# Kernel tuning notes

Measured on AMD Instinct MI355X. Metric: run time of the kernel, lower is better.

Reference implementation:

```python
import jax, jax.numpy as jnp
import numpy as np

TOP_K = 2

def setup_inputs() -> dict:
    key = jax.random.key(0)
    ks = jax.random.split(key, 5)
    B, S, H, F, E = 2, 1024, 2048, 4096, 8
    scale_h = 1.0 / np.sqrt(H)
    scale_f = 1.0 / np.sqrt(F)
    return {
        "hidden_states": jax.random.normal(ks[0], (B, S, H), dtype=jnp.float32),
        # nn.Linear weight layout is [out, in]
        "gate_w": jax.random.normal(ks[1], (E, H), dtype=jnp.float32) * scale_h,
        "w_gate": jax.random.normal(ks[2], (E, F, H), dtype=jnp.float32) * scale_h,
        "w_up": jax.random.normal(ks[3], (E, F, H), dtype=jnp.float32) * scale_h,
        "w_down": jax.random.normal(ks[4], (E, H, F), dtype=jnp.float32) * scale_f,
    }

def reference(hidden_states, gate_w, w_gate, w_up, w_down):
    B, S, H = hidden_states.shape
    E = gate_w.shape[0]
    x = hidden_states.reshape(-1, H)                     # [T, H]
    T = x.shape[0]
    # Router: softmax -> top-k -> renormalize
    router_logits = x @ gate_w.T                         # [T, E]
    routing_weights = jax.nn.softmax(router_logits, axis=-1)
    topk_w, topk_i = jax.lax.top_k(routing_weights, TOP_K)  # [T, k]
    topk_w = topk_w / jnp.sum(topk_w, axis=-1, keepdims=True)
    # Dense [T, E] combine weights (zero for non-selected experts);
    # equivalent math to the per-expert gather/scatter loop.
    dense_w = jnp.zeros((T, E), dtype=x.dtype).at[
        jnp.arange(T)[:, None], topk_i].set(topk_w)
    # SwiGLU experts, batched over E (grouped GEMM expressed densely)
    g = jnp.einsum('th,efh->tef', x, w_gate)             # [T, E, F]
    u = jnp.einsum('th,efh->tef', x, w_up)               # [T, E, F]
    h = jax.nn.silu(g) * u                               # [T, E, F]
    y = jnp.einsum('tef,ehf->teh', h, w_down)            # [T, E, H]
    out = jnp.einsum('te,teh->th', dense_w, y)           # [T, H]
    return out.reshape(B, S, H)
```

## Files before the change

### kernel.cpp

```cpp
#include <hip/hip_runtime.h>
#include <hip/hip_bf16.h>


#define T_TOK 2048
#define H_DIM 2048
#define F_DIM 4096
#define E_NUM 8
#define NPAIR (T_TOK * 2)

typedef __attribute__((ext_vector_type(8))) short short8;
typedef __attribute__((ext_vector_type(4))) float f32x4;

__device__ __forceinline__ unsigned short f2bf(float f) {
    unsigned u = __builtin_bit_cast(unsigned, f);
    u = (u + 0x7FFFu + ((u >> 16) & 1u)) >> 16;
    return (unsigned short)u;
}

__device__ __forceinline__ uint4 pack8(float4 a, float4 b) {
    uint4 o;
    o.x = f2bf(a.x) | ((unsigned)f2bf(a.y) << 16);
    o.y = f2bf(a.z) | ((unsigned)f2bf(a.w) << 16);
    o.z = f2bf(b.x) | ((unsigned)f2bf(b.y) << 16);
    o.w = f2bf(b.z) | ((unsigned)f2bf(b.w) << 16);
    return o;
}

__global__ void k_cvt_x(const float* __restrict__ x, ushort* __restrict__ xb) {
    int i = blockIdx.x * blockDim.x + threadIdx.x;
    const float4* p = (const float4*)x + (size_t)i * 2;
    ((uint4*)xb)[i] = pack8(p[0], p[1]);
}

__global__ void k_router(const float* __restrict__ x, const float* __restrict__ gw,
                         int2* __restrict__ eidx, float2* __restrict__ ew,
                         int* __restrict__ cnt) {
    int t = blockIdx.x * 4 + (threadIdx.x >> 6);
    int lane = threadIdx.x & 63;
    const float* xr = x + (size_t)t * H_DIM;
    float l[E_NUM];
    #pragma unroll
    for (int e = 0; e < E_NUM; e++) {
        const float* wr = gw + (size_t)e * H_DIM;
        float acc = 0.f;
        for (int i = lane; i < H_DIM; i += 64) acc += xr[i] * wr[i];
        #pragma unroll
        for (int o = 32; o; o >>= 1) acc += __shfl_xor(acc, o);
        l[e] = acc;
    }
    if (lane == 0) {
        int e0 = 0;
        #pragma unroll
        for (int e = 1; e < E_NUM; e++) if (l[e] > l[e0]) e0 = e;
        int e1 = -1;
        #pragma unroll
        for (int e = 0; e < E_NUM; e++) {
            if (e == e0) continue;
            if (e1 < 0 || l[e] > l[e1]) e1 = e;
        }
        float s1 = expf(l[e1] - l[e0]);
        float w0 = 1.f / (1.f + s1);
        float w1 = s1 * w0;
        eidx[t] = make_int2(e0, e1);
        ew[t]   = make_float2(w0, w1);
        atomicAdd(&cnt[e0], 1);
        atomicAdd(&cnt[e1], 1);
    }
}

__global__ void k_off(const int* __restrict__ cnt, int* __restrict__ off,
                      int* __restrict__ cnt2) {
    if (threadIdx.x == 0) {
        int s = 0;
        for (int e = 0; e < E_NUM; e++) { off[e] = s; s += cnt[e]; cnt2[e] = 0; }
        off[E_NUM] = s;
    }
}

__global__ void k_fill(const int2* __restrict__ eidx, const float2* __restrict__ ew,
                       const int* __restrict__ off, int* __restrict__ cnt2,
                       int* __restrict__ ptok, int2* __restrict__ inv) {
    int t = blockIdx.x * blockDim.x + threadIdx.x;
    if (t >= T_TOK) return;
    int2 e = eidx[t];
    int p0 = off[e.x] + atomicAdd(&cnt2[e.x], 1);
    ptok[p0] = t;
    int p1 = off[e.y] + atomicAdd(&cnt2[e.y], 1);
    ptok[p1] = t;
    inv[t] = make_int2(p0, p1);
}

__global__ __launch_bounds__(512, 4) void k_gemm1(
        const ushort* __restrict__ xb, const float* __restrict__ wg,
        const float* __restrict__ wu, const int* __restrict__ ptok,
        const int* __restrict__ off, ushort* __restrict__ hbuf) {
    __shared__ __align__(16) ushort As[256 * 64];
    __shared__ __align__(16) ushort Bg[64 * 64];
    __shared__ __align__(16) ushort Bu[64 * 64];

    int e = blockIdx.y >> 4, mt = blockIdx.y & 15;
    int base = off[e], ne = off[e + 1] - base;
    int row0 = mt * 256;
    if (row0 >= ne) return;
    int nb = blockIdx.x * 64;

    int tid = threadIdx.x;
    int wv = tid >> 6, l = tid & 63;
    int lr = l & 15, lk = l >> 4;
    int wm = wv >> 1, wn = wv & 1;

    int arow = tid >> 1, ah = (tid & 1) * 4;
    int p = base + min(row0 + arow, ne - 1);
    const ushort* xrow = xb + (size_t)ptok[p] * H_DIM;
    int asw = (arow & 7) << 4;
    int ao[4];
    #pragma unroll
    for (int j = 0; j < 4; j++)
        ao[j] = arow * 64 + ((((ah + j) * 16) ^ asw) >> 1);

    int brow = tid >> 3, bs = tid & 7;
    const float* wgrow = wg + ((size_t)e * F_DIM + nb + brow) * H_DIM + bs * 8;
    const float* wurow = wu + ((size_t)e * F_DIM + nb + brow) * H_DIM + bs * 8;
    int bo = brow * 64 + (((bs * 16) ^ ((brow & 7) << 4)) >> 1);

    int rsw = (lr & 7) << 4;

    f32x4 accg[4][2] = {}; f32x4 accu[4][2] = {};

    for (int kb = 0; kb < H_DIM; kb += 64) {
        __syncthreads();
        #pragma unroll
        for (int j = 0; j < 4; j++)
            *(uint4*)(&As[ao[j]]) = *(const uint4*)(xrow + kb + (ah + j) * 8);
        float4 g0 = *(const float4*)(wgrow + kb);
        float4 g1 = *(const float4*)(wgrow + kb + 4);
        *(uint4*)(&Bg[bo]) = pack8(g0, g1);
        float4 u0 = *(const float4*)(wurow + kb);
        float4 u1 = *(const float4*)(wurow + kb + 4);
        *(uint4*)(&Bu[bo]) = pack8(u0, u1);
        __syncthreads();

        #pragma unroll
        for (int kk = 0; kk < 2; kk++) {
            int kby = kk * 64 + lk * 16;
            short8 a[4];
            #pragma unroll
            for (int m = 0; m < 4; m++) {
                int row = wm * 64 + m * 16 + lr;
                a[m] = *(const short8*)(&As[(row * 128 + (kby ^ rsw)) >> 1]);
            }
            #pragma unroll
            for (int n = 0; n < 2; n++) {
                int rowb = wn * 32 + n * 16 + lr;
                int boff = (rowb * 128 + (kby ^ rsw)) >> 1;
                short8 bg8 = *(const short8*)(&Bg[boff]);
                short8 bu8 = *(const short8*)(&Bu[boff]);
                #pragma unroll
                for (int m = 0; m < 4; m++) {
                    accg[m][n] = __builtin_amdgcn_mfma_f32_16x16x32_bf16(a[m], bg8, accg[m][n], 0, 0, 0);
                    accu[m][n] = __builtin_amdgcn_mfma_f32_16x16x32_bf16(a[m], bu8, accu[m][n], 0, 0, 0);
                }
            }
        }
    }

    #pragma unroll
    for (int m = 0; m < 4; m++) {
        #pragma unroll
        for (int r = 0; r < 4; r++) {
            int lrow = wm * 64 + m * 16 + lk * 4 + r;
            if (row0 + lrow < ne) {
                size_t rb = (size_t)(base + row0 + lrow) * F_DIM + nb;
                #pragma unroll
                for (int n = 0; n < 2; n++) {
                    float g = accg[m][n][r], u = accu[m][n][r];
                    float hv = g / (1.f + __expf(-g)) * u;
                    hbuf[rb + wn * 32 + n * 16 + lr] = f2bf(hv);
                }
            }
        }
    }
}

__global__ __launch_bounds__(512, 2) void k_gemm2(
        const ushort* __restrict__ hbuf, const float* __restrict__ wd,
        const int* __restrict__ off, float* __restrict__ ybuf) {
    __shared__ __align__(16) ushort As[256 * 64];
    __shared__ __align__(16) ushort Bs[128 * 64];

    int e = blockIdx.y >> 3, mt = blockIdx.y & 7;
    int base = off[e], ne = off[e + 1] - base;
    int row0 = mt * 256;
    if (row0 >= ne) return;
    int nb = blockIdx.x * 128;

    int tid = threadIdx.x;
    int wv = tid >> 6, l = tid & 63;
    int lr = l & 15, lk = l >> 4;
    int wm = wv >> 1, wn = wv & 1;

    int arow = tid >> 1, ah = (tid & 1) * 4;
    int p = base + min(row0 + arow, ne - 1);
    const ushort* hrow = hbuf + (size_t)p * F_DIM;
    int asw = (arow & 7) << 4;
    int ao[4];
    #pragma unroll
    for (int j = 0; j < 4; j++)
        ao[j] = arow * 64 + ((((ah + j) * 16) ^ asw) >> 1);

    int brow = tid >> 2, bs = tid & 3;
    const float* wdrow = wd + ((size_t)e * H_DIM + nb + brow) * F_DIM + bs * 16;
    int bsw = (brow & 7) << 4;
    int bo0 = brow * 64 + (((bs * 32) ^ bsw) >> 1);
    int bo1 = brow * 64 + (((bs * 32 + 16) ^ bsw) >> 1);

    int rsw = (lr & 7) << 4;

    f32x4 acc[4][4] = {};

    for (int kb = 0; kb < F_DIM; kb += 64) {
        __syncthreads();
        #pragma unroll
        for (int j = 0; j < 4; j++)
            *(uint4*)(&As[ao[j]]) = *(const uint4*)(hrow + kb + (ah + j) * 8);
        float4 b0 = *(const float4*)(wdrow + kb);
        float4 b1 = *(const float4*)(wdrow + kb + 4);
        float4 b2 = *(const float4*)(wdrow + kb + 8);
        float4 b3 = *(const float4*)(wdrow + kb + 12);
        *(uint4*)(&Bs[bo0]) = pack8(b0, b1);
        *(uint4*)(&Bs[bo1]) = pack8(b2, b3);
        __syncthreads();

        #pragma unroll
        for (int kk = 0; kk < 2; kk++) {
            int kby = kk * 64 + lk * 16;
            short8 a[4];
            #pragma unroll
            for (int m = 0; m < 4; m++) {
                int row = wm * 64 + m * 16 + lr;
                a[m] = *(const short8*)(&As[(row * 128 + (kby ^ rsw)) >> 1]);
            }
            #pragma unroll
            for (int n = 0; n < 4; n++) {
                int rowb = wn * 64 + n * 16 + lr;
                short8 b8 = *(const short8*)(&Bs[(rowb * 128 + (kby ^ rsw)) >> 1]);
                #pragma unroll
                for (int m = 0; m < 4; m++)
                    acc[m][n] = __builtin_amdgcn_mfma_f32_16x16x32_bf16(a[m], b8, acc[m][n], 0, 0, 0);
            }
        }
    }

    #pragma unroll
    for (int m = 0; m < 4; m++) {
        #pragma unroll
        for (int r = 0; r < 4; r++) {
            int lrow = wm * 64 + m * 16 + lk * 4 + r;
            if (row0 + lrow < ne) {
                float* yrow = ybuf + (size_t)(base + row0 + lrow) * H_DIM + nb;
                #pragma unroll
                for (int n = 0; n < 4; n++)
                    yrow[wn * 64 + n * 16 + lr] = acc[m][n][r];
            }
        }
    }
}

__global__ void k_combine(const float* __restrict__ ybuf,
                          const float2* __restrict__ ew,
                          const int2* __restrict__ inv,
                          float* __restrict__ out) {
    int t = blockIdx.x;
    float2 w = ew[t];
    int2 pp = inv[t];
    const float4* y0 = (const float4*)(ybuf + (size_t)pp.x * H_DIM);
    const float4* y1 = (const float4*)(ybuf + (size_t)pp.y * H_DIM);
    float4* o = (float4*)(out + (size_t)t * H_DIM);
    for (int j = threadIdx.x; j < H_DIM / 4; j += blockDim.x) {
        float4 a = y0[j], b = y1[j];
        float4 r;
        r.x = w.x * a.x + w.y * b.x;
        r.y = w.x * a.y + w.y * b.y;
        r.z = w.x * a.z + w.y * b.z;
        r.w = w.x * a.w + w.y * b.w;
        o[j] = r;
    }
}

extern "C" void kernel_launch(void* const* d_in, const int* in_sizes, int n_in,
                              void* d_out, int out_size, void* d_ws, size_t ws_size,
                              hipStream_t stream) {
    const float* x  = (const float*)d_in[0];
    const float* gw = (const float*)d_in[1];
    const float* wg = (const float*)d_in[2];
    const float* wu = (const float*)d_in[3];
    const float* wd = (const float*)d_in[4];
    float* out = (float*)d_out;

    char* ws = (char*)d_ws;
    size_t o = 0;
    ushort* xb   = (ushort*)(ws + o); o += (size_t)T_TOK * H_DIM * 2;
    ushort* hbuf = (ushort*)(ws + o); o += (size_t)NPAIR * F_DIM * 2;
    float*  ybuf = (float*) (ws + o); o += (size_t)NPAIR * H_DIM * 4;
    int*    ptok = (int*)   (ws + o); o += NPAIR * 4;
    int2*   eidx = (int2*)  (ws + o); o += T_TOK * 8;
    float2* ew   = (float2*)(ws + o); o += T_TOK * 8;
    int2*   inv  = (int2*)  (ws + o); o += T_TOK * 8;
    int*    cnt  = (int*)   (ws + o); o += 256;
    int*    cnt2 = (int*)   (ws + o); o += 256;
    int*    off  = (int*)   (ws + o); o += 256;

    hipMemsetAsync(cnt, 0, 256, stream);

    k_cvt_x <<<T_TOK * H_DIM / 8 / 256, 256, 0, stream>>>(x, xb);
    k_router<<<T_TOK / 4, 256, 0, stream>>>(x, gw, eidx, ew, cnt);
    k_off   <<<1, 64, 0, stream>>>(cnt, off, cnt2);
    k_fill  <<<T_TOK / 256, 256, 0, stream>>>(eidx, ew, off, cnt2, ptok, inv);

    dim3 g1(F_DIM / 64, E_NUM * 16);
    k_gemm1<<<g1, 512, 0, stream>>>(xb, wg, wu, ptok, off, hbuf);
    dim3 g2(H_DIM / 128, E_NUM * 8);
    k_gemm2<<<g2, 512, 0, stream>>>(hbuf, wd, off, ybuf);
    k_combine<<<T_TOK, 256, 0, stream>>>(ybuf, ew, inv, out);
}
```

Before: 592.2 us.

## Remap GEMM grids to 1D XCD-aware order grouping each expert per XCD

Both expert GEMMs now use a flat 1D grid. The block id is remapped so that each group of consecutive blocks sent to the same XCD covers one expert. Within that group the M-tiles that share a weight column tile run next to each other, so the fp32 weight tiles should be reused from that XCD's L2 instead of being spread across chiplets. The gemm1 grid also drops the always-empty M-tiles beyond 2048 rows. The risk is load imbalance between XCDs when experts receive uneven token counts. The x-conversion kernel's packing is also split into two 4-wide halves.

New measurement: 710.1 us. +19.9%, slower.

```diff
diff --git a/kernel.cpp b/kernel.cpp
--- a/kernel.cpp
+++ b/kernel.cpp
@@ -26,10 +26,18 @@
     return o;
 }
 
+__device__ __forceinline__ uint2 pack4(float4 a) {
+    uint2 o;
+    o.x = f2bf(a.x) | ((unsigned)f2bf(a.y) << 16);
+    o.y = f2bf(a.z) | ((unsigned)f2bf(a.w) << 16);
+    return o;
+}
+
 __global__ void k_cvt_x(const float* __restrict__ x, ushort* __restrict__ xb) {
     int i = blockIdx.x * blockDim.x + threadIdx.x;
     const float4* p = (const float4*)x + (size_t)i * 2;
-    ((uint4*)xb)[i] = pack8(p[0], p[1]);
+    uint2 lo = pack4(p[0]), hi = pack4(p[1]);
+    ((uint4*)xb)[i] = make_uint4(lo.x, lo.y, hi.x, hi.y);
 }
 
 __global__ void k_router(const float* __restrict__ x, const float* __restrict__ gw,
@@ -98,11 +106,16 @@
     __shared__ __align__(16) ushort Bg[64 * 64];
     __shared__ __align__(16) ushort Bu[64 * 64];
 
-    int e = blockIdx.y >> 4, mt = blockIdx.y & 15;
+    int bid = blockIdx.x;
+    int orig = (bid & 7) * 512 + (bid >> 3);
+    int mt = orig & 7;
+    int nbt = (orig >> 3) & 63;
+    int e = orig >> 9;
+
     int base = off[e], ne = off[e + 1] - base;
     int row0 = mt * 256;
     if (row0 >= ne) return;
-    int nb = blockIdx.x * 64;
+    int nb = nbt * 64;
 
     int tid = threadIdx.x;
     int wv = tid >> 6, l = tid & 63;
@@ -188,11 +201,16 @@
     __shared__ __align__(16) ushort As[256 * 64];
     __shared__ __align__(16) ushort Bs[128 * 64];
 
-    int e = blockIdx.y >> 3, mt = blockIdx.y & 7;
+    int bid = blockIdx.x;
+    int orig = (bid & 7) * 128 + (bid >> 3);
+    int mt = orig & 7;
+    int nbt = (orig >> 3) & 15;
+    int e = orig >> 7;
+
     int base = off[e], ne = off[e + 1] - base;
     int row0 = mt * 256;
     if (row0 >= ne) return;
-    int nb = blockIdx.x * 128;
+    int nb = nbt * 128;
 
     int tid = threadIdx.x;
     int wv = tid >> 6, l = tid & 63;
@@ -317,9 +335,7 @@
     k_off   <<<1, 64, 0, stream>>>(cnt, off, cnt2);
     k_fill  <<<T_TOK / 256, 256, 0, stream>>>(eidx, ew, off, cnt2, ptok, inv);
 
-    dim3 g1(F_DIM / 64, E_NUM * 16);
-    k_gemm1<<<g1, 512, 0, stream>>>(xb, wg, wu, ptok, off, hbuf);
-    dim3 g2(H_DIM / 128, E_NUM * 8);
-    k_gemm2<<<g2, 512, 0, stream>>>(hbuf, wd, off, ybuf);
+    k_gemm1<<<4096, 512, 0, stream>>>(xb, wg, wu, ptok, off, hbuf);
+    k_gemm2<<<1024, 512, 0, stream>>>(hbuf, wd, off, ybuf);
     k_combine<<<T_TOK, 256, 0, stream>>>(ybuf, ew, inv, out);
 }
```

## Split fused gate/up GEMM into two passes with wider N tiles

Applied to the files above, without the earlier changes.

The fused gate+up GEMM, which used 64-column tiles and two accumulator sets, is replaced by a templated single-weight GEMM with 128-column tiles, launched twice. The first pass writes gate pre-activations in bf16 into hbuf. The second pass reads them back, applies SiLU, and multiplies by the up result. The aim is to cut register pressure and reuse each A tile across more N columns. In exchange, the A tile and token gather are loaded twice, hbuf takes an extra global read and write, and the gate value is rounded to bf16 before SiLU. The x conversion helper is also reorganised cosmetically.

Result: slower. 669.4 us (+13.0%).

```diff
diff --git a/kernel.cpp b/kernel.cpp
--- a/kernel.cpp
+++ b/kernel.cpp
@@ -15,6 +15,11 @@
     unsigned u = __builtin_bit_cast(unsigned, f);
     u = (u + 0x7FFFu + ((u >> 16) & 1u)) >> 16;
     return (unsigned short)u;
+}
+
+__device__ __forceinline__ float bf2f(unsigned short us) {
+    unsigned u = ((unsigned)us) << 16;
+    return __builtin_bit_cast(float, u);
 }
 
 __device__ __forceinline__ uint4 pack8(float4 a, float4 b) {
@@ -26,10 +31,18 @@
     return o;
 }
 
+__device__ __forceinline__ uint2 pack4(float4 a) {
+    uint2 o;
+    o.x = f2bf(a.x) | ((unsigned)f2bf(a.y) << 16);
+    o.y = f2bf(a.z) | ((unsigned)f2bf(a.w) << 16);
+    return o;
+}
+
 __global__ void k_cvt_x(const float* __restrict__ x, ushort* __restrict__ xb) {
     int i = blockIdx.x * blockDim.x + threadIdx.x;
     const float4* p = (const float4*)x + (size_t)i * 2;
-    ((uint4*)xb)[i] = pack8(p[0], p[1]);
+    uint2 lo = pack4(p[0]), hi = pack4(p[1]);
+    ((uint4*)xb)[i] = make_uint4(lo.x, lo.y, hi.x, hi.y);
 }
 
 __global__ void k_router(const float* __restrict__ x, const float* __restrict__ gw,
@@ -90,19 +103,19 @@
     inv[t] = make_int2(p0, p1);
 }
 
-__global__ __launch_bounds__(512, 4) void k_gemm1(
-        const ushort* __restrict__ xb, const float* __restrict__ wg,
-        const float* __restrict__ wu, const int* __restrict__ ptok,
-        const int* __restrict__ off, ushort* __restrict__ hbuf) {
+template <int FUSE>
+__global__ __launch_bounds__(512, 2) void k_gemm1t(
+        const ushort* __restrict__ xb, const float* __restrict__ w,
+        const int* __restrict__ ptok, const int* __restrict__ off,
+        ushort* __restrict__ hbuf) {
     __shared__ __align__(16) ushort As[256 * 64];
-    __shared__ __align__(16) ushort Bg[64 * 64];
-    __shared__ __align__(16) ushort Bu[64 * 64];
-
-    int e = blockIdx.y >> 4, mt = blockIdx.y & 15;
+    __shared__ __align__(16) ushort Bs[128 * 64];
+
+    int e = blockIdx.y >> 3, mt = blockIdx.y & 7;
     int base = off[e], ne = off[e + 1] - base;
     int row0 = mt * 256;
     if (row0 >= ne) return;
-    int nb = blockIdx.x * 64;
+    int nb = blockIdx.x * 128;
 
     int tid = threadIdx.x;
     int wv = tid >> 6, l = tid & 63;
@@ -118,26 +131,27 @@
     for (int j = 0; j < 4; j++)
         ao[j] = arow * 64 + ((((ah + j) * 16) ^ asw) >> 1);
 
-    int brow = tid >> 3, bs = tid & 7;
-    const float* wgrow = wg + ((size_t)e * F_DIM + nb + brow) * H_DIM + bs * 8;
-    const float* wurow = wu + ((size_t)e * F_DIM + nb + brow) * H_DIM + bs * 8;
-    int bo = brow * 64 + (((bs * 16) ^ ((brow & 7) << 4)) >> 1);
+    int brow = tid >> 2, bs = tid & 3;
+    const float* wrow = w + ((size_t)e * F_DIM + nb + brow) * H_DIM + bs * 16;
+    int bsw = (brow & 7) << 4;
+    int bo0 = brow * 64 + (((bs * 32) ^ bsw) >> 1);
+    int bo1 = brow * 64 + (((bs * 32 + 16) ^ bsw) >> 1);
 
     int rsw = (lr & 7) << 4;
 
-    f32x4 accg[4][2] = {}; f32x4 accu[4][2] = {};
+    f32x4 acc[4][4] = {};
 
     for (int kb = 0; kb < H_DIM; kb += 64) {
         __syncthreads();
         #pragma unroll
         for (int j = 0; j < 4; j++)
             *(uint4*)(&As[ao[j]]) = *(const uint4*)(xrow + kb + (ah + j) * 8);
-        float4 g0 = *(const float4*)(wgrow + kb);
-        float4 g1 = *(const float4*)(wgrow + kb + 4);
-        *(uint4*)(&Bg[bo]) = pack8(g0, g1);
-        float4 u0 = *(const float4*)(wurow + kb);
-        float4 u1 = *(const float4*)(wurow + kb + 4);
-        *(uint4*)(&Bu[bo]) = pack8(u0, u1);
+        float4 b0 = *(const float4*)(wrow + kb);
+        float4 b1 = *(const float4*)(wrow + kb + 4);
+        float4 b2 = *(const float4*)(wrow + kb + 8);
+        float4 b3 = *(const float4*)(wrow + kb + 12);
+        *(uint4*)(&Bs[bo0]) = pack8(b0, b1);
+        *(uint4*)(&Bs[bo1]) = pack8(b2, b3);
         __syncthreads();
 
         #pragma unroll
@@ -150,16 +164,12 @@
                 a[m] = *(const short8*)(&As[(row * 128 + (kby ^ rsw)) >> 1]);
             }
             #pragma unroll
-            for (int n = 0; n < 2; n++) {
-                int rowb = wn * 32 + n * 16 + lr;
-                int boff = (rowb * 128 + (kby ^ rsw)) >> 1;
-                short8 bg8 = *(const short8*)(&Bg[boff]);
-                short8 bu8 = *(const short8*)(&Bu[boff]);
+            for (int n = 0; n < 4; n++) {
+                int rowb = wn * 64 + n * 16 + lr;
+                short8 b8 = *(const short8*)(&Bs[(rowb * 128 + (kby ^ rsw)) >> 1]);
                 #pragma unroll
-                for (int m = 0; m < 4; m++) {
-                    accg[m][n] = __builtin_amdgcn_mfma_f32_16x16x32_bf16(a[m], bg8, accg[m][n], 0, 0, 0);
-                    accu[m][n] = __builtin_amdgcn_mfma_f32_16x16x32_bf16(a[m], bu8, accu[m][n], 0, 0, 0);
-                }
+                for (int m = 0; m < 4; m++)
+                    acc[m][n] = __builtin_amdgcn_mfma_f32_16x16x32_bf16(a[m], b8, acc[m][n], 0, 0, 0);
             }
         }
     }
@@ -170,12 +180,18 @@
         for (int r = 0; r < 4; r++) {
             int lrow = wm * 64 + m * 16 + lk * 4 + r;
             if (row0 + lrow < ne) {
-                size_t rb = (size_t)(base + row0 + lrow) * F_DIM + nb;
+                ushort* hb = hbuf + (size_t)(base + row0 + lrow) * F_DIM + nb;
                 #pragma unroll
-                for (int n = 0; n < 2; n++) {
-                    float g = accg[m][n][r], u = accu[m][n][r];
-                    float hv = g / (1.f + __expf(-g)) * u;
-                    hbuf[rb + wn * 32 + n * 16 + lr] = f2bf(hv);
+                for (int n = 0; n < 4; n++) {
+                    int col = wn * 64 + n * 16 + lr;
+                    if (FUSE) {
+                        float g = bf2f(hb[col]);
+                        float u = acc[m][n][r];
+                        float hv = g / (1.f + __expf(-g)) * u;
+                        hb[col] = f2bf(hv);
+                    } else {
+                        hb[col] = f2bf(acc[m][n][r]);
+                    }
                 }
             }
         }
@@ -317,8 +333,9 @@
     k_off   <<<1, 64, 0, stream>>>(cnt, off, cnt2);
     k_fill  <<<T_TOK / 256, 256, 0, stream>>>(eidx, ew, off, cnt2, ptok, inv);
 
-    dim3 g1(F_DIM / 64, E_NUM * 16);
-    k_gemm1<<<g1, 512, 0, stream>>>(xb, wg, wu, ptok, off, hbuf);
+    dim3 g1(F_DIM / 128, E_NUM * 8);
+    k_gemm1t<0><<<g1, 512, 0, stream>>>(xb, wg, ptok, off, hbuf);
+    k_gemm1t<1><<<g1, 512, 0, stream>>>(xb, wu, ptok, off, hbuf);
     dim3 g2(H_DIM / 128, E_NUM * 8);
     k_gemm2<<<g2, 512, 0, stream>>>(hbuf, wd, off, ybuf);
     k_combine<<<T_TOK, 256, 0, stream>>>(ybuf, ew, inv, out);
```
